# Kernel tuning notes

Measured on AMD Instinct MI355X. Metric: run time of the kernel, lower is better.

The kernel has to match this reference:

```python
import jax, jax.numpy as jnp
import numpy as np

E, K, H, I = 8, 2, 768, 1152  # experts, top_k, hidden, intermediate
T = 4096  # total tokens


def setup_inputs() -> dict:
    key = jax.random.key(0)
    ks = jax.random.split(key, 6)
    return {
        "x": jax.random.normal(ks[0], (T, H), jnp.float32),
        "gate_w": jax.random.normal(ks[1], (E, H), jnp.float32) * 0.02,
        "correction_bias": jnp.zeros((E,), jnp.float32),
        "Wi": jax.random.normal(ks[2], (E, H, 2 * I), jnp.float32) * 0.02,
        "Wo": jax.random.normal(ks[3], (E, I, H), jnp.float32) * 0.02,
        "shared_Wi": jax.random.normal(ks[4], (2 * I, H), jnp.float32) * 0.02,
        "shared_Wo": jax.random.normal(ks[5], (H, I), jnp.float32) * 0.02,
    }


def reference(x, gate_w, correction_bias, Wi, Wo, shared_Wi, shared_Wo):
    # ---- shared SwiGLU expert (dropout=0 in eval) ----
    sh = x @ shared_Wi.T                      # (T, 2I)
    s_in, s_gate = sh[:, :I], sh[:, I:]
    shared_out = (jax.nn.silu(s_in) * s_gate) @ shared_Wo.T  # (T, H)

    # ---- sigmoid top-k router with bias correction ----
    logits = jax.nn.sigmoid(x @ gate_w.T)     # (T, E)
    sel = logits + correction_bias
    _, indices = jax.lax.top_k(sel, K)        # (T, K)
    weights = jnp.take_along_axis(logits, indices, axis=-1)  # bias-free scores
    weights = weights / jnp.sum(weights, axis=-1, keepdims=True)

    # combine weight per (expert, token): cw[e, t] = sum_k weights[t,k]*[indices[t,k]==e]
    one_hot = jax.nn.one_hot(indices, E, dtype=x.dtype)      # (T, K, E)
    cw = jnp.einsum("tke,tk->et", one_hot, weights)          # (E, T)

    # ---- experts: SwiGLU per expert, weighted scatter-combine ----
    h = jnp.einsum("th,ehf->etf", x, Wi)      # (E, T, 2I)
    proj, gate = h[..., :I], h[..., I:]
    act = jax.nn.silu(gate) * proj            # (E, T, I)
    act = act * cw[:, :, None]                # fold combine weights before Wo
    expert_out = jnp.einsum("eti,eih->th", act, Wo)          # (T, H)

    return expert_out + shared_out
```

## Files before the change

kernel.cpp:

```cpp
#include <hip/hip_runtime.h>
#include <stdint.h>

#define E_  8
#define H_  768
#define I_  1152
#define T_  4096
#define F2_ (2*I_)

typedef unsigned short u16;
typedef __attribute__((ext_vector_type(8))) __bf16 bf16x8;
typedef __attribute__((ext_vector_type(4))) float floatx4;

typedef const void __attribute__((address_space(1))) as1_void;
typedef void __attribute__((address_space(3))) as3_void;

__device__ __forceinline__ void gld16(void* lds, const void* g) {
  __builtin_amdgcn_global_load_lds((as1_void*)g, (as3_void*)lds, 16, 0, 0);
}

__device__ __forceinline__ u16 f2bf(float f) {
  union { float f; unsigned int i; } v; v.f = f;
  unsigned int r = v.i + 0x7FFF + ((v.i >> 16) & 1);
  return (u16)(r >> 16);
}

#define GATE_BLKS (T_ / 4)
#define CONV_BLKS ((F2_ * H_ + H_ * I_) / 1024)
#define TWI_X (F2_ / 64)
#define TWI_Y (H_ / 64)
#define TWI_BLKS (TWI_X * TWI_Y * E_)
#define TWO_X (H_ / 64)
#define TWO_Y (I_ / 64)
#define TWO_BLKS (TWO_X * TWO_Y * E_)
#define PREP_BLKS (GATE_BLKS + CONV_BLKS + TWI_BLKS + TWO_BLKS)

__device__ __forceinline__ void transpose_role(const float* __restrict__ src,
                                               u16* __restrict__ dst,
                                               int R, int C, int xi, int yi, int zi) {
  __shared__ u16 tile[64][65];
  const float* s = src + (long)zi * R * C;
  u16*         d = dst + (long)zi * R * C;
  int r0 = yi * 64, c0 = xi * 64;
  int tx = threadIdx.x & 63, ty = threadIdx.x >> 6;
  #pragma unroll
  for (int k = 0; k < 64; k += 4)
    tile[ty + k][tx] = f2bf(s[(long)(r0 + ty + k) * C + (c0 + tx)]);
  __syncthreads();
  #pragma unroll
  for (int k = 0; k < 64; k += 4)
    d[(long)(c0 + ty + k) * R + (r0 + tx)] = tile[tx][ty + k];
}

__global__ __launch_bounds__(256)
void prep_all(const float* __restrict__ x, const float* __restrict__ gw,
              const float* __restrict__ bias,
              int* __restrict__ top2e, float* __restrict__ top2w, u16* __restrict__ xb,
              const float* __restrict__ sWi, u16* __restrict__ sWib,
              const float* __restrict__ sWo, u16* __restrict__ sWob,
              const float* __restrict__ Wi, u16* __restrict__ WiT,
              const float* __restrict__ Wo, u16* __restrict__ WoT) {
  int b = blockIdx.x;
  if (b < GATE_BLKS) {
    int t    = b * 4 + (threadIdx.x >> 6);
    int lane = threadIdx.x & 63;
    float acc[E_];
    #pragma unroll
    for (int e = 0; e < E_; e++) acc[e] = 0.f;
    #pragma unroll
    for (int i = 0; i < H_ / 256; i++) {
      int c = i * 256 + lane * 4;
      float4 xv = *(const float4*)(x + (long)t * H_ + c);
      ushort4 u;
      u.x = f2bf(xv.x); u.y = f2bf(xv.y); u.z = f2bf(xv.z); u.w = f2bf(xv.w);
      *(ushort4*)(xb + (long)t * H_ + c) = u;
      #pragma unroll
      for (int e = 0; e < E_; e++) {
        float4 g = *(const float4*)(gw + e * H_ + c);
        acc[e] += xv.x * g.x + xv.y * g.y + xv.z * g.z + xv.w * g.w;
      }
    }
    #pragma unroll
    for (int e = 0; e < E_; e++) {
      #pragma unroll
      for (int s = 32; s > 0; s >>= 1) acc[e] += __shfl_xor(acc[e], s);
    }
    if (lane == 0) {
      float logits[E_], sel[E_];
      #pragma unroll
      for (int e = 0; e < E_; e++) {
        logits[e] = 1.f / (1.f + expf(-acc[e]));
        sel[e]    = logits[e] + bias[e];
      }
      int i0 = 0;
      #pragma unroll
      for (int e = 1; e < E_; e++) if (sel[e] > sel[i0]) i0 = e;
      int i1 = (i0 == 0) ? 1 : 0;
      #pragma unroll
      for (int e = 0; e < E_; e++) if (e != i0 && sel[e] > sel[i1]) i1 = e;
      float w0 = logits[i0], w1 = logits[i1], s = w0 + w1;
      top2e[t * 2 + 0] = i0;  top2w[t * 2 + 0] = w0 / s;
      top2e[t * 2 + 1] = i1;  top2w[t * 2 + 1] = w1 / s;
    }
  } else if (b < GATE_BLKS + CONV_BLKS) {
    int i = ((b - GATE_BLKS) * 256 + threadIdx.x) * 4;
    const int n1 = F2_ * H_;
    const float* s; u16* d;
    if (i < n1) { s = sWi + i; d = sWib + i; }
    else        { s = sWo + (i - n1); d = sWob + (i - n1); }
    float4 v = *(const float4*)s;
    ushort4 u;
    u.x = f2bf(v.x); u.y = f2bf(v.y); u.z = f2bf(v.z); u.w = f2bf(v.w);
    *(ushort4*)d = u;
  } else if (b < GATE_BLKS + CONV_BLKS + TWI_BLKS) {
    int i = b - (GATE_BLKS + CONV_BLKS);
    int xi = i % TWI_X, yi = (i / TWI_X) % TWI_Y, zi = i / (TWI_X * TWI_Y);
    transpose_role(Wi, WiT, H_, F2_, xi, yi, zi);
  } else {
    int i = b - (GATE_BLKS + CONV_BLKS + TWI_BLKS);
    int xi = i % TWO_X, yi = (i / TWO_X) % TWO_Y, zi = i / (TWO_X * TWO_Y);
    transpose_role(Wo, WoT, I_, H_, xi, yi, zi);
  }
}

__global__ void build_lists(const int* __restrict__ top2e, const float* __restrict__ top2w,
                            int* __restrict__ counts, int* __restrict__ offs,
                            int* __restrict__ list, float* __restrict__ wlist,
                            int* __restrict__ pos) {
  __shared__ int scnt[4][E_];
  __shared__ int sq[4];
  __shared__ int soffs[E_];
  int e = blockIdx.x;
  int tid = threadIdx.x, w = tid >> 6, lane = tid & 63;
  const int Q = (2 * T_) / 4;

  int c8[E_];
  #pragma unroll
  for (int q = 0; q < E_; q++) c8[q] = 0;
  for (int i = tid; i < 2 * T_; i += 256) {
    int v = top2e[i];
    #pragma unroll
    for (int q = 0; q < E_; q++) c8[q] += (v == q);
  }
  int qstart = w * Q;
  int ce = 0;
  for (int i = qstart + lane; i < qstart + Q; i += 64) ce += (top2e[i] == e);
  #pragma unroll
  for (int q = 0; q < E_; q++)
    #pragma unroll
    for (int s = 32; s > 0; s >>= 1) c8[q] += __shfl_xor(c8[q], s);
  #pragma unroll
  for (int s = 32; s > 0; s >>= 1) ce += __shfl_xor(ce, s);
  if (lane == 0) {
    #pragma unroll
    for (int q = 0; q < E_; q++) scnt[w][q] = c8[q];
    sq[w] = ce;
  }
  __syncthreads();
  if (tid == 0) {
    int s = 0;
    #pragma unroll
    for (int q = 0; q < E_; q++) {
      int tot = scnt[0][q] + scnt[1][q] + scnt[2][q] + scnt[3][q];
      soffs[q] = s;
      if (e == 0) { counts[q] = tot; offs[q] = s; }
      s += tot;
    }
    if (e == 0) { counts[8] = T_; offs[8] = 2 * T_; }
  }
  __syncthreads();
  int base = soffs[e];
  #pragma unroll
  for (int w2 = 0; w2 < 4; w2++) if (w2 < w) base += sq[w2];
  unsigned long long lt = (lane == 63) ? (~0ull >> 1) : ((1ull << lane) - 1);
  for (int i0 = qstart; i0 < qstart + Q; i0 += 64) {
    int s = i0 + lane;
    bool m = (top2e[s] == e);
    unsigned long long mask = __ballot(m);
    if (m) {
      int p = base + __popcll(mask & lt);
      list[p]  = s >> 1;
      wlist[p] = top2w[s];
      pos[s]   = p;
    }
    base += __popcll(mask);
  }
  for (int t = e * (T_ / 8) + tid; t < (e + 1) * (T_ / 8); t += 256) {
    list[2 * T_ + t]  = t;
    wlist[2 * T_ + t] = 1.f;
  }
}

#define PP1 168
__global__ __launch_bounds__(256, 2)
void gemm_act_all(const u16* __restrict__ A, const u16* __restrict__ WiT,
                  const u16* __restrict__ sWib, u16* __restrict__ act,
                  const int* __restrict__ list, const float* __restrict__ wlist,
                  const int* __restrict__ counts, const int* __restrict__ offsets) {
  __shared__ __align__(16) u16 As[128 * 64];
  __shared__ __align__(16) u16 Bs[2][64 * 64];

  int id = blockIdx.x;
  int y  = id / PP1, p = id - y * PP1;
  if (p >= 162) return;
  int z = p / 18, xblk = p - z * 18;

  int cnt = counts[z], off = offsets[z];
  int row0 = y * 128;
  if (row0 >= cnt) return;
  const u16* B = (z == 8) ? sWib : (WiT + (long)z * F2_ * H_);
  int n0 = xblk * 64;

  int tid  = threadIdx.x;
  int lane = tid & 63, wv = tid >> 6;
  int wr   = wv >> 1, wc = wv & 1;
  int half = lane & 15, quad = lane >> 4;

  int rA  = tid >> 3;
  int lc8 = ((tid & 7) ^ (rA & 7)) * 8;
  const u16* ap[4];
  #pragma unroll
  for (int n = 0; n < 4; n++) {
    int rr = min(row0 + rA + n * 32, cnt - 1);
    ap[n] = A + (long)list[off + rr] * H_ + lc8;
  }
  const u16* bp[2][2];
  #pragma unroll
  for (int h = 0; h < 2; h++)
    #pragma unroll
    for (int m = 0; m < 2; m++)
      bp[h][m] = B + (long)(h * I_ + n0 + m * 32 + rA) * H_ + lc8;

  floatx4 acc[2][4][2];
  #pragma unroll
  for (int q = 0; q < 2; q++)
    #pragma unroll
    for (int i = 0; i < 4; i++)
      #pragma unroll
      for (int j = 0; j < 2; j++) acc[q][i][j] = (floatx4)0.f;

  for (int k0 = 0; k0 < H_; k0 += 64) {
    if (k0) __syncthreads();
    #pragma unroll
    for (int n = 0; n < 4; n++) gld16(As + (n * 256 + tid) * 8, ap[n] + k0);
    #pragma unroll
    for (int h = 0; h < 2; h++)
      #pragma unroll
      for (int m = 0; m < 2; m++) gld16(Bs[h] + (m * 256 + tid) * 8, bp[h][m] + k0);
    __syncthreads();
    #pragma unroll
    for (int kk = 0; kk < 2; kk++) {
      int cs = ((kk * 4 + quad) ^ (half & 7)) * 8;
      bf16x8 a[4], bq[2][2];
      #pragma unroll
      for (int i = 0; i < 4; i++)
        a[i] = *(const bf16x8*)(As + (wr * 64 + i * 16 + half) * 64 + cs);
      #pragma unroll
      for (int q = 0; q < 2; q++)
        #pragma unroll
        for (int j = 0; j < 2; j++)
          bq[q][j] = *(const bf16x8*)(Bs[q] + (wc * 32 + j * 16 + half) * 64 + cs);
      #pragma unroll
      for (int i = 0; i < 4; i++)
        #pragma unroll
        for (int q = 0; q < 2; q++)
          #pragma unroll
          for (int j = 0; j < 2; j++)
            acc[q][i][j] = __builtin_amdgcn_mfma_f32_16x16x32_bf16(a[i], bq[q][j], acc[q][i][j], 0, 0, 0);
    }
  }

  bool sh = (z == 8);
  #pragma unroll
  for (int i = 0; i < 4; i++) {
    #pragma unroll
    for (int r = 0; r < 4; r++) {
      int g = row0 + wr * 64 + i * 16 + quad * 4 + r;
      if (g < cnt) {
        float w = wlist[off + g];
        #pragma unroll
        for (int j = 0; j < 2; j++) {
          float va = acc[0][i][j][r];
          float vb = acc[1][i][j][r];
          float zz = sh ? va : vb;
          float o  = sh ? vb : va;
          float sg = zz / (1.f + expf(-zz));
          float v  = sg * o * w;
          int col  = n0 + wc * 32 + j * 16 + half;
          act[(long)(off + g) * I_ + col] = f2bf(v);
        }
      }
    }
  }
}

#define PP2 56
__global__ __launch_bounds__(256, 4)
void gemm_out_all(const u16* __restrict__ A, const u16* __restrict__ WoT,
                  const u16* __restrict__ sWob, float* __restrict__ out,
                  float* __restrict__ eobuf,
                  const int* __restrict__ counts, const int* __restrict__ offsets) {
  __shared__ __align__(16) u16 As[64 * 64];
  __shared__ __align__(16) u16 Bs[128 * 64];

  int id = blockIdx.x;
  int y  = id / PP2, p = id - y * PP2;
  if (p >= 54) return;
  int z = p / 6, xblk = p - z * 6;

  int cnt = counts[z], off = offsets[z];
  int row0 = y * 64;
  if (row0 >= cnt) return;
  const u16* B = (z == 8) ? sWob : (WoT + (long)z * H_ * I_);
  int n0 = xblk * 128;

  int tid  = threadIdx.x;
  int lane = tid & 63, wv = tid >> 6;
  int wr   = wv >> 1, wc = wv & 1;
  int half = lane & 15, quad = lane >> 4;

  int rA  = tid >> 3;
  int lc8 = ((tid & 7) ^ (rA & 7)) * 8;
  const u16* ap[2];
  #pragma unroll
  for (int n = 0; n < 2; n++) {
    long rr = off + min(row0 + rA + n * 32, cnt - 1);
    ap[n] = A + rr * I_ + lc8;
  }
  const u16* bp[4];
  #pragma unroll
  for (int m = 0; m < 4; m++)
    bp[m] = B + (long)(n0 + m * 32 + rA) * I_ + lc8;

  floatx4 acc[2][4];
  #pragma unroll
  for (int i = 0; i < 2; i++)
    #pragma unroll
    for (int j = 0; j < 4; j++) acc[i][j] = (floatx4)0.f;

  for (int k0 = 0; k0 < I_; k0 += 64) {
    if (k0) __syncthreads();
    #pragma unroll
    for (int n = 0; n < 2; n++) gld16(As + (n * 256 + tid) * 8, ap[n] + k0);
    #pragma unroll
    for (int m = 0; m < 4; m++) gld16(Bs + (m * 256 + tid) * 8, bp[m] + k0);
    __syncthreads();
    #pragma unroll
    for (int kk = 0; kk < 2; kk++) {
      int cs = ((kk * 4 + quad) ^ (half & 7)) * 8;
      bf16x8 a[2], b[4];
      #pragma unroll
      for (int i = 0; i < 2; i++)
        a[i] = *(const bf16x8*)(As + (wr * 32 + i * 16 + half) * 64 + cs);
      #pragma unroll
      for (int j = 0; j < 4; j++)
        b[j] = *(const bf16x8*)(Bs + (wc * 64 + j * 16 + half) * 64 + cs);
      #pragma unroll
      for (int i = 0; i < 2; i++)
        #pragma unroll
        for (int j = 0; j < 4; j++)
          acc[i][j] = __builtin_amdgcn_mfma_f32_16x16x32_bf16(a[i], b[j], acc[i][j], 0, 0, 0);
    }
  }

  bool sh = (z == 8);
  #pragma unroll
  for (int i = 0; i < 2; i++) {
    #pragma unroll
    for (int r = 0; r < 4; r++) {
      int g = row0 + wr * 32 + i * 16 + quad * 4 + r;
      if (g < cnt) {
        float* orow = sh ? (out + (long)g * H_) : (eobuf + (long)(off + g) * H_);
        #pragma unroll
        for (int j = 0; j < 4; j++) {
          int col = n0 + wc * 64 + j * 16 + half;
          orow[col] = acc[i][j][r];
        }
      }
    }
  }
}

__global__ void final_reduce(float* __restrict__ out, const float* __restrict__ eobuf,
                             const int* __restrict__ pos) {
  int gid = blockIdx.x * 256 + threadIdx.x;
  int t = gid / (H_ / 4), c = (gid % (H_ / 4)) * 4;
  int p0 = pos[t * 2], p1 = pos[t * 2 + 1];
  float4 a = *(const float4*)(out   + (long)t  * H_ + c);
  float4 b = *(const float4*)(eobuf + (long)p0 * H_ + c);
  float4 d = *(const float4*)(eobuf + (long)p1 * H_ + c);
  a.x += b.x + d.x; a.y += b.y + d.y; a.z += b.z + d.z; a.w += b.w + d.w;
  *(float4*)(out + (long)t * H_ + c) = a;
}

extern "C" void kernel_launch(void* const* d_in, const int* in_sizes, int n_in,
                              void* d_out, int out_size, void* d_ws, size_t ws_size,
                              hipStream_t stream) {
  const float* x      = (const float*)d_in[0];
  const float* gate_w = (const float*)d_in[1];
  const float* bias   = (const float*)d_in[2];
  const float* Wi     = (const float*)d_in[3];
  const float* Wo     = (const float*)d_in[4];
  const float* sWi    = (const float*)d_in[5];
  const float* sWo    = (const float*)d_in[6];
  float* out          = (float*)d_out;

  char* ws = (char*)d_ws;
  size_t o = 0;
  auto alloc = [&](size_t bytes) -> void* {
    o = (o + 255) & ~(size_t)255;
    void* p = ws + o;
    o += bytes;
    return p;
  };
  u16*   xb    = (u16*)  alloc((size_t)T_ * H_ * 2);
  u16*   sWib  = (u16*)  alloc((size_t)F2_ * H_ * 2);
  u16*   sWob  = (u16*)  alloc((size_t)H_ * I_ * 2);
  u16*   WiT   = (u16*)  alloc((size_t)E_ * F2_ * H_ * 2);
  u16*   WoT   = (u16*)  alloc((size_t)E_ * H_ * I_ * 2);
  u16*   act   = (u16*)  alloc((size_t)3 * T_ * I_ * 2);
  int*   top2e = (int*)  alloc((size_t)T_ * 2 * 4);
  float* top2w = (float*)alloc((size_t)T_ * 2 * 4);
  int*   count = (int*)  alloc(9 * 4);
  int*   offs  = (int*)  alloc(9 * 4);
  int*   list  = (int*)  alloc((size_t)3 * T_ * 4);
  float* wlist = (float*)alloc((size_t)3 * T_ * 4);
  int*   pos   = (int*)  alloc((size_t)2 * T_ * 4);
  float* eobuf = (float*)WiT;

  prep_all<<<PREP_BLKS, 256, 0, stream>>>(x, gate_w, bias, top2e, top2w, xb,
                                          sWi, sWib, sWo, sWob, Wi, WiT, Wo, WoT);
  build_lists<<<E_, 256, 0, stream>>>(top2e, top2w, count, offs, list, wlist, pos);

  gemm_act_all<<<32 * PP1, 256, 0, stream>>>(xb, WiT, sWib, act, list, wlist, count, offs);
  gemm_out_all<<<64 * PP2, 256, 0, stream>>>(act, WoT, sWob, out, eobuf, count, offs);
  final_reduce<<<(T_ * (H_ / 4)) / 256, 256, 0, stream>>>(out, eobuf, pos);
}
```

Before: 297.6 us.

## Scatter expert outputs with atomics, widen out-GEMM tile, vectorize weight transpose

```diff
diff --git a/kernel.cpp b/kernel.cpp
--- a/kernel.cpp
+++ b/kernel.cpp
@@ -32,23 +32,37 @@
 #define TWO_X (H_ / 64)
 #define TWO_Y (I_ / 64)
 #define TWO_BLKS (TWO_X * TWO_Y * E_)
-#define PREP_BLKS (GATE_BLKS + CONV_BLKS + TWI_BLKS + TWO_BLKS)
+#define ZOUT_BLKS ((T_ * H_) / 1024)
+#define PREP_BLKS (GATE_BLKS + CONV_BLKS + TWI_BLKS + TWO_BLKS + ZOUT_BLKS)
 
 __device__ __forceinline__ void transpose_role(const float* __restrict__ src,
                                                u16* __restrict__ dst,
                                                int R, int C, int xi, int yi, int zi) {
-  __shared__ u16 tile[64][65];
+  __shared__ u16 tile[64][68];
   const float* s = src + (long)zi * R * C;
   u16*         d = dst + (long)zi * R * C;
   int r0 = yi * 64, c0 = xi * 64;
-  int tx = threadIdx.x & 63, ty = threadIdx.x >> 6;
-  #pragma unroll
-  for (int k = 0; k < 64; k += 4)
-    tile[ty + k][tx] = f2bf(s[(long)(r0 + ty + k) * C + (c0 + tx)]);
+  int c4 = (threadIdx.x & 15) * 4;
+  int rr = threadIdx.x >> 4;
+  #pragma unroll
+  for (int k = 0; k < 64; k += 16) {
+    float4 v = *(const float4*)(s + (long)(r0 + rr + k) * C + (c0 + c4));
+    ushort4 u;
+    u.x = f2bf(v.x); u.y = f2bf(v.y); u.z = f2bf(v.z); u.w = f2bf(v.w);
+    *(ushort4*)&tile[rr + k][c4] = u;
+  }
   __syncthreads();
-  #pragma unroll
-  for (int k = 0; k < 64; k += 4)
-    d[(long)(c0 + ty + k) * R + (r0 + tx)] = tile[tx][ty + k];
+  int c  = threadIdx.x >> 2;
+  int rq = (threadIdx.x & 3) * 4;
+  #pragma unroll
+  for (int k = 0; k < 64; k += 16) {
+    ushort4 u;
+    u.x = tile[rq + k + 0][c];
+    u.y = tile[rq + k + 1][c];
+    u.z = tile[rq + k + 2][c];
+    u.w = tile[rq + k + 3][c];
+    *(ushort4*)(d + (long)(c0 + c) * R + (r0 + rq + k)) = u;
+  }
 }
 
 __global__ __launch_bounds__(256)
@@ -58,7 +72,8 @@
               const float* __restrict__ sWi, u16* __restrict__ sWib,
               const float* __restrict__ sWo, u16* __restrict__ sWob,
               const float* __restrict__ Wi, u16* __restrict__ WiT,
-              const float* __restrict__ Wo, u16* __restrict__ WoT) {
+              const float* __restrict__ Wo, u16* __restrict__ WoT,
+              float* __restrict__ out) {
   int b = blockIdx.x;
   if (b < GATE_BLKS) {
     int t    = b * 4 + (threadIdx.x >> 6);
@@ -115,17 +130,20 @@
     int i = b - (GATE_BLKS + CONV_BLKS);
     int xi = i % TWI_X, yi = (i / TWI_X) % TWI_Y, zi = i / (TWI_X * TWI_Y);
     transpose_role(Wi, WiT, H_, F2_, xi, yi, zi);
-  } else {
+  } else if (b < GATE_BLKS + CONV_BLKS + TWI_BLKS + TWO_BLKS) {
     int i = b - (GATE_BLKS + CONV_BLKS + TWI_BLKS);
     int xi = i % TWO_X, yi = (i / TWO_X) % TWO_Y, zi = i / (TWO_X * TWO_Y);
     transpose_role(Wo, WoT, I_, H_, xi, yi, zi);
+  } else {
+    int i = ((b - (GATE_BLKS + CONV_BLKS + TWI_BLKS + TWO_BLKS)) * 256 + threadIdx.x) * 4;
+    float4 z; z.x = z.y = z.z = z.w = 0.f;
+    *(float4*)(out + i) = z;
   }
 }
 
 __global__ void build_lists(const int* __restrict__ top2e, const float* __restrict__ top2w,
                             int* __restrict__ counts, int* __restrict__ offs,
-                            int* __restrict__ list, float* __restrict__ wlist,
-                            int* __restrict__ pos) {
+                            int* __restrict__ list, float* __restrict__ wlist) {
   __shared__ int scnt[4][E_];
   __shared__ int sq[4];
   __shared__ int soffs[E_];
@@ -180,7 +198,6 @@
       int p = base + __popcll(mask & lt);
       list[p]  = s >> 1;
       wlist[p] = top2w[s];
-      pos[s]   = p;
     }
     base += __popcll(mask);
   }
@@ -293,25 +310,25 @@
   }
 }
 
-#define PP2 56
+#define PP2 40
 __global__ __launch_bounds__(256, 4)
 void gemm_out_all(const u16* __restrict__ A, const u16* __restrict__ WoT,
                   const u16* __restrict__ sWob, float* __restrict__ out,
-                  float* __restrict__ eobuf,
+                  const int* __restrict__ list,
                   const int* __restrict__ counts, const int* __restrict__ offsets) {
   __shared__ __align__(16) u16 As[64 * 64];
-  __shared__ __align__(16) u16 Bs[128 * 64];
+  __shared__ __align__(16) u16 Bs[192 * 64];
 
   int id = blockIdx.x;
   int y  = id / PP2, p = id - y * PP2;
-  if (p >= 54) return;
-  int z = p / 6, xblk = p - z * 6;
+  if (p >= 36) return;
+  int z = p / 4, xblk = p - z * 4;
 
   int cnt = counts[z], off = offsets[z];
   int row0 = y * 64;
   if (row0 >= cnt) return;
   const u16* B = (z == 8) ? sWob : (WoT + (long)z * H_ * I_);
-  int n0 = xblk * 128;
+  int n0 = xblk * 192;
 
   int tid  = threadIdx.x;
   int lane = tid & 63, wv = tid >> 6;
@@ -326,70 +343,58 @@
     long rr = off + min(row0 + rA + n * 32, cnt - 1);
     ap[n] = A + rr * I_ + lc8;
   }
-  const u16* bp[4];
-  #pragma unroll
-  for (int m = 0; m < 4; m++)
+  const u16* bp[6];
+  #pragma unroll
+  for (int m = 0; m < 6; m++)
     bp[m] = B + (long)(n0 + m * 32 + rA) * I_ + lc8;
 
-  floatx4 acc[2][4];
+  floatx4 acc[2][6];
   #pragma unroll
   for (int i = 0; i < 2; i++)
     #pragma unroll
-    for (int j = 0; j < 4; j++) acc[i][j] = (floatx4)0.f;
+    for (int j = 0; j < 6; j++) acc[i][j] = (floatx4)0.f;
 
   for (int k0 = 0; k0 < I_; k0 += 64) {
     if (k0) __syncthreads();
     #pragma unroll
     for (int n = 0; n < 2; n++) gld16(As + (n * 256 + tid) * 8, ap[n] + k0);
     #pragma unroll
-    for (int m = 0; m < 4; m++) gld16(Bs + (m * 256 + tid) * 8, bp[m] + k0);
+    for (int m = 0; m < 6; m++) gld16(Bs + (m * 256 + tid) * 8, bp[m] + k0);
     __syncthreads();
     #pragma unroll
     for (int kk = 0; kk < 2; kk++) {
       int cs = ((kk * 4 + quad) ^ (half & 7)) * 8;
-      bf16x8 a[2], b[4];
+      bf16x8 a[2], b[6];
       #pragma unroll
       for (int i = 0; i < 2; i++)
         a[i] = *(const bf16x8*)(As + (wr * 32 + i * 16 + half) * 64 + cs);
       #pragma unroll
-      for (int j = 0; j < 4; j++)
-        b[j] = *(const bf16x8*)(Bs + (wc * 64 + j * 16 + half) * 64 + cs);
+      for (int j = 0; j < 6; j++)
+        b[j] = *(const bf16x8*)(Bs + (wc * 96 + j * 16 + half) * 64 + cs);
       #pragma unroll
       for (int i = 0; i < 2; i++)
         #pragma unroll
-        for (int j = 0; j < 4; j++)
+        for (int j = 0; j < 6; j++)
           acc[i][j] = __builtin_amdgcn_mfma_f32_16x16x32_bf16(a[i], b[j], acc[i][j], 0, 0, 0);
     }
   }
 
-  bool sh = (z == 8);
   #pragma unroll
   for (int i = 0; i < 2; i++) {
     #pragma unroll
     for (int r = 0; r < 4; r++) {
       int g = row0 + wr * 32 + i * 16 + quad * 4 + r;
       if (g < cnt) {
-        float* orow = sh ? (out + (long)g * H_) : (eobuf + (long)(off + g) * H_);
+        int token = list[off + g];
+        float* orow = out + (long)token * H_;
         #pragma unroll
-        for (int j = 0; j < 4; j++) {
-          int col = n0 + wc * 64 + j * 16 + half;
-          orow[col] = acc[i][j][r];
+        for (int j = 0; j < 6; j++) {
+          int col = n0 + wc * 96 + j * 16 + half;
+          atomicAdd(orow + col, acc[i][j][r]);
         }
       }
     }
   }
-}
-
-__global__ void final_reduce(float* __restrict__ out, const float* __restrict__ eobuf,
-                             const int* __restrict__ pos) {
-  int gid = blockIdx.x * 256 + threadIdx.x;
-  int t = gid / (H_ / 4), c = (gid % (H_ / 4)) * 4;
-  int p0 = pos[t * 2], p1 = pos[t * 2 + 1];
-  float4 a = *(const float4*)(out   + (long)t  * H_ + c);
-  float4 b = *(const float4*)(eobuf + (long)p0 * H_ + c);
-  float4 d = *(const float4*)(eobuf + (long)p1 * H_ + c);
-  a.x += b.x + d.x; a.y += b.y + d.y; a.z += b.z + d.z; a.w += b.w + d.w;
-  *(float4*)(out + (long)t * H_ + c) = a;
 }
 
 extern "C" void kernel_launch(void* const* d_in, const int* in_sizes, int n_in,
@@ -424,14 +429,11 @@
   int*   offs  = (int*)  alloc(9 * 4);
   int*   list  = (int*)  alloc((size_t)3 * T_ * 4);
   float* wlist = (float*)alloc((size_t)3 * T_ * 4);
-  int*   pos   = (int*)  alloc((size_t)2 * T_ * 4);
-  float* eobuf = (float*)WiT;
 
   prep_all<<<PREP_BLKS, 256, 0, stream>>>(x, gate_w, bias, top2e, top2w, xb,
-                                          sWi, sWib, sWo, sWob, Wi, WiT, Wo, WoT);
-  build_lists<<<E_, 256, 0, stream>>>(top2e, top2w, count, offs, list, wlist, pos);
+                                          sWi, sWib, sWo, sWob, Wi, WiT, Wo, WoT, out);
+  build_lists<<<E_, 256, 0, stream>>>(top2e, top2w, count, offs, list, wlist);
 
   gemm_act_all<<<32 * PP1, 256, 0, stream>>>(xb, WiT, sWib, act, list, wlist, count, offs);
-  gemm_out_all<<<64 * PP2, 256, 0, stream>>>(act, WoT, sWob, out, eobuf, count, offs);
-  final_reduce<<<(T_ * (H_ / 4)) / 256, 256, 0, stream>>>(out, eobuf, pos);
-}
+  gemm_out_all<<<64 * PP2, 256, 0, stream>>>(act, WoT, sWob, out, list, count, offs);
+}
```

Result: no change. 301.4 us (+1.3%).
